# Optimization experiments

Hardware: AMD Instinct MI355X
Metric: run time of the kernel (lower is better)

The kernel has to match this reference:

```python
import jax, jax.numpy as jnp
import numpy as np

B, NT, NZ, CIN, H, DOUT, L = 16, 128, 256, 3, 64, 128, 3
N = NT * NZ  # 32768 nodes
EPS = 1e-5


def _build_edges():
    # Toroidal grid: each node connects to 4 neighbors (wrap-around in theta and zeta).
    T, Z = np.meshgrid(np.arange(NT), np.arange(NZ), indexing='ij')
    curr = (T * NZ + Z).ravel()
    nbrs = np.stack([
        (((T + 1) % NT) * NZ + Z).ravel(),
        (((T - 1) % NT) * NZ + Z).ravel(),
        (T * NZ + (Z + 1) % NZ).ravel(),
        (T * NZ + (Z - 1) % NZ).ravel(),
    ], axis=1)
    src = np.repeat(curr, 4)
    dst = nbrs.ravel()
    return np.stack([src, dst]).astype(np.int32)  # (2, 4N)


def setup_inputs() -> dict:
    key = jax.random.key(0)
    ks = jax.random.split(key, 8)
    s = lambda k, shp, fan: jax.random.normal(k, shp, jnp.float32) / np.float32(np.sqrt(fan))
    return {
        'x': jax.random.normal(ks[0], (B, CIN, N), jnp.float32),
        'edge_index': jnp.asarray(_build_edges()),
        'embed_W': s(ks[1], (CIN, H), CIN),
        'embed_b': jnp.zeros((H,), jnp.float32),
        'mp_W1': s(ks[2], (L, 2 * H, H), 2 * H),
        'mp_b1': jnp.zeros((L, H), jnp.float32),
        'mp_g1': jnp.ones((L, H), jnp.float32),
        'mp_be1': jnp.zeros((L, H), jnp.float32),
        'mp_W2': s(ks[3], (L, H, H), H),
        'mp_b2': jnp.zeros((L, H), jnp.float32),
        'mp_g2': jnp.ones((L, H), jnp.float32),
        'mp_be2': jnp.zeros((L, H), jnp.float32),
        'head_W1': s(ks[4], (H, H), H),
        'head_b1': jnp.zeros((H,), jnp.float32),
        'head_W2': s(ks[5], (H, DOUT), H),
        'head_b2': jnp.zeros((DOUT,), jnp.float32),
    }


def _bn(y, g, b):
    # BatchNorm1d in training mode: biased batch stats over (batch*nodes).
    m = y.mean(axis=(0, 1))
    v = y.var(axis=(0, 1))
    return (y - m) * (g * jax.lax.rsqrt(v + EPS)) + b


def reference(x, edge_index, embed_W, embed_b, mp_W1, mp_b1, mp_g1, mp_be1,
              mp_W2, mp_b2, mp_g2, mp_be2, head_W1, head_b1, head_W2, head_b2):
    src, dst = edge_index[0], edge_index[1]
    # embedding: (B,3,N) -> (B,N,H)
    h = jax.nn.relu(jnp.einsum('bcn,ch->bnh', x, embed_W) + embed_b)
    deg = jnp.zeros((N,), x.dtype).at[dst].add(1.0)
    deg = jnp.clip(deg, 1.0)[None, :, None]  # (1,N,1), all 4 on this graph
    for l in range(L):
        # gather neighbor features and scatter-add to destination, mean aggregate
        agg = jnp.zeros_like(h).at[:, dst, :].add(h[:, src, :]) / deg
        comb = jnp.concatenate([h, agg], axis=-1)  # (B,N,2H)
        y = jax.nn.relu(_bn(comb @ mp_W1[l] + mp_b1[l], mp_g1[l], mp_be1[l]))
        y = jax.nn.relu(_bn(y @ mp_W2[l] + mp_b2[l], mp_g2[l], mp_be2[l]))
        h = y + h  # residual (c_in == c_out)
    pooled = h.mean(axis=1)  # AdaptiveAvgPool1d(1) over nodes
    return jax.nn.relu(pooled @ head_W1 + head_b1) @ head_W2 + head_b2
```

## Files before the change

kernel.cpp:

```cpp
#include <hip/hip_runtime.h>

typedef unsigned short u16;
typedef u16 u16x8 __attribute__((ext_vector_type(8)));
typedef short s16x8 __attribute__((ext_vector_type(8)));
typedef float f32x4 __attribute__((ext_vector_type(4)));

#define NNODES 32768
#define EPSV 1e-5f
#define INV_ROWS (1.0f / 524288.0f)

__device__ __forceinline__ float bf2f(u16 u) {
  union { unsigned int i; float f; } v; v.i = ((unsigned int)u) << 16; return v.f;
}
__device__ __forceinline__ u16 f2bf(float f) {
  union { float f; unsigned int i; } v; v.f = f;
  unsigned int r = v.i + 0x7FFFu + ((v.i >> 16) & 1u);
  return (u16)(r >> 16);
}

__global__ __launch_bounds__(256) void k_prep(
    const float* __restrict__ W1, const float* __restrict__ W2,
    u16* __restrict__ w1t, u16* __restrict__ w2t) {
  int idx = blockIdx.x * 256 + threadIdx.x;
  if (idx < 24576) {
    int l = idx >> 13, rem = idx & 8191;
    int n = rem >> 7, k = rem & 127;
    float w = W1[l * 8192 + k * 64 + n];
    if (k >= 64) w *= 0.25f;
    w1t[idx] = f2bf(w);
  } else {
    int idx2 = idx - 24576;
    if (idx2 < 12288) {
      int l = idx2 >> 12, rem = idx2 & 4095;
      int n = rem >> 6, k = rem & 63;
      w2t[idx2] = f2bf(W2[l * 4096 + k * 64 + n]);
    }
  }
}

__global__ __launch_bounds__(256) void k_embed(
    const float* __restrict__ x, const float* __restrict__ eW,
    const float* __restrict__ eb, u16* __restrict__ h) {
  int tid = threadIdx.x;
  int chunk = tid & 7;
  int r = blockIdx.x * 32 + (tid >> 3);
  int b = r >> 15;
  int n = r & 32767;
  const float* xb = x + (size_t)b * 3 * NNODES + n;
  float x0 = xb[0], x1 = xb[NNODES], x2 = xb[2 * NNODES];
  int c0 = chunk * 8;
  u16x8 ov;
#pragma unroll
  for (int j = 0; j < 8; ++j) {
    float acc = eb[c0 + j] + x0 * eW[c0 + j] + x1 * eW[64 + c0 + j] + x2 * eW[128 + c0 + j];
    ov[j] = f2bf(fmaxf(acc, 0.f));
  }
  *reinterpret_cast<u16x8*>(&h[(size_t)r * 64 + c0]) = ov;
}

#define RSTR 72
__global__ __launch_bounds__(256) void k_gemm1(
    const u16* __restrict__ h, u16* __restrict__ ybuf,
    const u16* __restrict__ w1t, const float* __restrict__ b1,
    float* __restrict__ sums) {
  __shared__ __align__(16) u16 s_self[130 * RSTR];
  __shared__ __align__(16) u16 s_tp[128 * RSTR];
  __shared__ __align__(16) u16 s_tm[128 * RSTR];
  __shared__ __align__(16) u16 t_s[4][16 * RSTR];
  __shared__ float stat_s[4][128];

  int tid = threadIdx.x;
  int wv = tid >> 6, ln = tid & 63, ln15 = ln & 15, quad = ln >> 4;
  int blk = blockIdx.x;
  int xcd = blk & 7;
  int j = blk >> 3;
  int b = j >> 5;
  int local = j & 31;
  int t = xcd * 16 + (local >> 1);
  int half = local & 1;
  int z0 = half * 128;
  const u16* hb = h + (((size_t)b) << 15) * 64;
  int tp = (t + 1) & 127, tm = (t + 127) & 127;

  s16x8 bfT[4][2], bfB[4][2];
#pragma unroll
  for (int c = 0; c < 4; ++c)
#pragma unroll
    for (int kk = 0; kk < 2; ++kk) {
      bfT[c][kk] = *reinterpret_cast<const s16x8*>(
          &w1t[(c * 16 + ln15) * 128 + kk * 32 + quad * 8]);
      bfB[c][kk] = *reinterpret_cast<const s16x8*>(
          &w1t[(c * 16 + ln15) * 128 + 64 + kk * 32 + quad * 8]);
    }

  {
    u16x8 va[7];
#pragma unroll
    for (int ii = 0; ii < 7; ++ii) {
      int i = tid + ii * 256;
      int c = i & 7;
      int r = (i >= 1040) ? ((i - 1040) >> 3) : (i >> 3);
      int ring_t = (i >= 1040) ? tp : t;
      int z = (i >= 1040) ? (z0 + r) : ((z0 + 255 + r) & 255);
      va[ii] = *reinterpret_cast<const u16x8*>(&hb[((size_t)(ring_t * 256 + z)) * 64 + c * 8]);
    }
#pragma unroll
    for (int ii = 0; ii < 7; ++ii) {
      int i = tid + ii * 256;
      int c = i & 7;
      if (i < 1040) {
        *reinterpret_cast<u16x8*>(&s_self[(i >> 3) * RSTR + c * 8]) = va[ii];
      } else {
        *reinterpret_cast<u16x8*>(&s_tp[((i - 1040) >> 3) * RSTR + c * 8]) = va[ii];
      }
    }
    u16x8 vb[6];
#pragma unroll
    for (int ii = 0; ii < 6; ++ii) {
      int i = tid + (ii + 7) * 256;
      if (i < 3088) {
        int c = i & 7;
        int r = (i < 2064) ? ((i - 1040) >> 3) : ((i - 2064) >> 3);
        int ring_t = (i < 2064) ? tp : tm;
        vb[ii] = *reinterpret_cast<const u16x8*>(
            &hb[((size_t)(ring_t * 256 + z0 + r)) * 64 + c * 8]);
      }
    }
#pragma unroll
    for (int ii = 0; ii < 6; ++ii) {
      int i = tid + (ii + 7) * 256;
      if (i < 3088) {
        int c = i & 7;
        if (i < 2064) {
          *reinterpret_cast<u16x8*>(&s_tp[((i - 1040) >> 3) * RSTR + c * 8]) = vb[ii];
        } else {
          *reinterpret_cast<u16x8*>(&s_tm[((i - 2064) >> 3) * RSTR + c * 8]) = vb[ii];
        }
      }
    }
  }

  float bias_c[4];
#pragma unroll
  for (int c = 0; c < 4; ++c) bias_c[c] = b1[c * 16 + ln15];

  __syncthreads();

  float ls[4] = {0.f, 0.f, 0.f, 0.f}, ls2[4] = {0.f, 0.f, 0.f, 0.f};
  u16* ts = &t_s[wv][0];
  int cA = quad * 8;

#pragma unroll
  for (int st = 0; st < 2; ++st) {
    int row0 = st * 64 + wv * 16;
    int lr = row0 + ln15;

    s16x8 s0  = *reinterpret_cast<const s16x8*>(&s_self[(lr + 1) * RSTR + cA]);
    s16x8 s1  = *reinterpret_cast<const s16x8*>(&s_self[(lr + 1) * RSTR + 32 + cA]);
    s16x8 n0a = *reinterpret_cast<const s16x8*>(&s_tp[lr * RSTR + cA]);
    s16x8 n0b = *reinterpret_cast<const s16x8*>(&s_tp[lr * RSTR + 32 + cA]);
    s16x8 n1a = *reinterpret_cast<const s16x8*>(&s_tm[lr * RSTR + cA]);
    s16x8 n1b = *reinterpret_cast<const s16x8*>(&s_tm[lr * RSTR + 32 + cA]);
    s16x8 n2a = *reinterpret_cast<const s16x8*>(&s_self[(lr + 2) * RSTR + cA]);
    s16x8 n2b = *reinterpret_cast<const s16x8*>(&s_self[(lr + 2) * RSTR + 32 + cA]);
    s16x8 n3a = *reinterpret_cast<const s16x8*>(&s_self[lr * RSTR + cA]);
    s16x8 n3b = *reinterpret_cast<const s16x8*>(&s_self[lr * RSTR + 32 + cA]);

    f32x4 acc[4];
#pragma unroll
    for (int c = 0; c < 4; ++c) acc[c] = (f32x4){0.f, 0.f, 0.f, 0.f};
#pragma unroll
    for (int c = 0; c < 4; ++c) {
      acc[c] = __builtin_amdgcn_mfma_f32_16x16x32_bf16(s0,  bfT[c][0], acc[c], 0, 0, 0);
      acc[c] = __builtin_amdgcn_mfma_f32_16x16x32_bf16(s1,  bfT[c][1], acc[c], 0, 0, 0);
      acc[c] = __builtin_amdgcn_mfma_f32_16x16x32_bf16(n0a, bfB[c][0], acc[c], 0, 0, 0);
      acc[c] = __builtin_amdgcn_mfma_f32_16x16x32_bf16(n0b, bfB[c][1], acc[c], 0, 0, 0);
      acc[c] = __builtin_amdgcn_mfma_f32_16x16x32_bf16(n1a, bfB[c][0], acc[c], 0, 0, 0);
      acc[c] = __builtin_amdgcn_mfma_f32_16x16x32_bf16(n1b, bfB[c][1], acc[c], 0, 0, 0);
      acc[c] = __builtin_amdgcn_mfma_f32_16x16x32_bf16(n2a, bfB[c][0], acc[c], 0, 0, 0);
      acc[c] = __builtin_amdgcn_mfma_f32_16x16x32_bf16(n2b, bfB[c][1], acc[c], 0, 0, 0);
      acc[c] = __builtin_amdgcn_mfma_f32_16x16x32_bf16(n3a, bfB[c][0], acc[c], 0, 0, 0);
      acc[c] = __builtin_amdgcn_mfma_f32_16x16x32_bf16(n3b, bfB[c][1], acc[c], 0, 0, 0);
    }

    __builtin_amdgcn_wave_barrier();
#pragma unroll
    for (int c = 0; c < 4; ++c)
#pragma unroll
      for (int rg = 0; rg < 4; ++rg) {
        float vy = acc[c][rg] + bias_c[c];
        ls[c] += vy;
        ls2[c] += vy * vy;
        ts[(quad * 4 + rg) * RSTR + c * 16 + ln15] = f2bf(vy);
      }
    __builtin_amdgcn_wave_barrier();
    size_t R0 = (((size_t)b) << 15) + (size_t)t * 256 + z0 + row0;
    int lr2 = ln >> 2;
#pragma unroll
    for (int p = 0; p < 2; ++p) {
      int ck = (ln & 3) + p * 4;
      u16x8 v = *reinterpret_cast<const u16x8*>(&ts[lr2 * RSTR + ck * 8]);
      *reinterpret_cast<u16x8*>(&ybuf[(R0 + lr2) * 64 + ck * 8]) = v;
    }
    __builtin_amdgcn_wave_barrier();
  }

#pragma unroll
  for (int c = 0; c < 4; ++c) {
    ls[c]  += __shfl_xor(ls[c], 16, 64);  ls[c]  += __shfl_xor(ls[c], 32, 64);
    ls2[c] += __shfl_xor(ls2[c], 16, 64); ls2[c] += __shfl_xor(ls2[c], 32, 64);
  }
  if (ln < 16) {
#pragma unroll
    for (int c = 0; c < 4; ++c) {
      stat_s[wv][c * 16 + ln] = ls[c];
      stat_s[wv][64 + c * 16 + ln] = ls2[c];
    }
  }
  __syncthreads();
  if (tid < 128) {
    float s = stat_s[0][tid] + stat_s[1][tid] + stat_s[2][tid] + stat_s[3][tid];
    atomicAdd(&sums[xcd * 128 + tid], s);
  }
}

__global__ __launch_bounds__(256) void k_gemm2(
    u16* __restrict__ ybuf, const u16* __restrict__ w2t,
    const float* __restrict__ b2, const float* __restrict__ sums1,
    const float* __restrict__ g1, const float* __restrict__ be1,
    float* __restrict__ sums2) {
  __shared__ __align__(16) u16 t_s[4][16 * RSTR];
  __shared__ float s1_s[64], sh1_s[64];
  __shared__ float stat_s[4][128];

  int tid = threadIdx.x;
  int wv = tid >> 6, ln = tid & 63, ln15 = ln & 15, quad = ln >> 4;

  if (tid < 64) {
    float s = 0.f, s2 = 0.f;
#pragma unroll
    for (int sl = 0; sl < 8; ++sl) { s += sums1[sl * 128 + tid]; s2 += sums1[sl * 128 + 64 + tid]; }
    float m = s * INV_ROWS;
    float v = s2 * INV_ROWS - m * m;
    float sc = g1[tid] * rsqrtf(v + EPSV);
    s1_s[tid] = sc;
    sh1_s[tid] = be1[tid] - m * sc;
  }

  s16x8 bf[4][2];
#pragma unroll
  for (int c = 0; c < 4; ++c)
#pragma unroll
    for (int kk = 0; kk < 2; ++kk)
      bf[c][kk] = *reinterpret_cast<const s16x8*>(
          &w2t[(c * 16 + ln15) * 64 + kk * 32 + quad * 8]);

  float bias_c[4];
#pragma unroll
  for (int c = 0; c < 4; ++c) bias_c[c] = b2[c * 16 + ln15];

  __syncthreads();

  float sA[2][8], shA[2][8];
#pragma unroll
  for (int kk = 0; kk < 2; ++kk)
#pragma unroll
    for (int j = 0; j < 8; ++j) {
      int ch = kk * 32 + quad * 8 + j;
      sA[kk][j] = s1_s[ch];
      shA[kk][j] = sh1_s[ch];
    }

  float ls[4] = {0.f, 0.f, 0.f, 0.f}, ls2[4] = {0.f, 0.f, 0.f, 0.f};
  u16* ts = &t_s[wv][0];

  auto ld2 = [&](int it, u16x8* Y) {
    size_t row = (size_t)blockIdx.x * 256 + it * 64 + wv * 16 + ln15;
    Y[0] = *reinterpret_cast<const u16x8*>(&ybuf[row * 64 + quad * 8]);
    Y[1] = *reinterpret_cast<const u16x8*>(&ybuf[row * 64 + 32 + quad * 8]);
  };

  auto consume2 = [&](int it, u16x8* Y) {
    s16x8 a0, a1;
#pragma unroll
    for (int j = 0; j < 8; ++j) {
      a0[j] = (short)f2bf(fmaxf(bf2f(Y[0][j]) * sA[0][j] + shA[0][j], 0.f));
      a1[j] = (short)f2bf(fmaxf(bf2f(Y[1][j]) * sA[1][j] + shA[1][j], 0.f));
    }
    f32x4 acc[4];
#pragma unroll
    for (int c = 0; c < 4; ++c) acc[c] = (f32x4){0.f, 0.f, 0.f, 0.f};
#pragma unroll
    for (int c = 0; c < 4; ++c) {
      acc[c] = __builtin_amdgcn_mfma_f32_16x16x32_bf16(a0, bf[c][0], acc[c], 0, 0, 0);
      acc[c] = __builtin_amdgcn_mfma_f32_16x16x32_bf16(a1, bf[c][1], acc[c], 0, 0, 0);
    }
    __builtin_amdgcn_wave_barrier();
#pragma unroll
    for (int c = 0; c < 4; ++c)
#pragma unroll
      for (int rg = 0; rg < 4; ++rg) {
        float vy = acc[c][rg] + bias_c[c];
        ls[c] += vy;
        ls2[c] += vy * vy;
        ts[(quad * 4 + rg) * RSTR + c * 16 + ln15] = f2bf(vy);
      }
    __builtin_amdgcn_wave_barrier();
    size_t r0 = (size_t)blockIdx.x * 256 + it * 64 + wv * 16;
    int lr = ln >> 2;
#pragma unroll
    for (int p = 0; p < 2; ++p) {
      int ck = (ln & 3) + p * 4;
      u16x8 v = *reinterpret_cast<const u16x8*>(&ts[lr * RSTR + ck * 8]);
      *reinterpret_cast<u16x8*>(&ybuf[(r0 + lr) * 64 + ck * 8]) = v;
    }
    __builtin_amdgcn_wave_barrier();
  };

  u16x8 YA[2], YB[2];
  ld2(0, YA);
#pragma unroll 1
  for (int it = 0; it < 4; it += 2) {
    ld2(it + 1, YB);
    consume2(it, YA);
    if (it + 2 < 4) ld2(it + 2, YA);
    consume2(it + 1, YB);
  }

#pragma unroll
  for (int c = 0; c < 4; ++c) {
    ls[c]  += __shfl_xor(ls[c], 16, 64);  ls[c]  += __shfl_xor(ls[c], 32, 64);
    ls2[c] += __shfl_xor(ls2[c], 16, 64); ls2[c] += __shfl_xor(ls2[c], 32, 64);
  }
  if (ln < 16) {
#pragma unroll
    for (int c = 0; c < 4; ++c) {
      stat_s[wv][c * 16 + ln] = ls[c];
      stat_s[wv][64 + c * 16 + ln] = ls2[c];
    }
  }
  __syncthreads();
  if (tid < 128) {
    float s = stat_s[0][tid] + stat_s[1][tid] + stat_s[2][tid] + stat_s[3][tid];
    atomicAdd(&sums2[(blockIdx.x & 7) * 128 + tid], s);
  }
}

__global__ __launch_bounds__(256) void k_resid(
    u16* __restrict__ h, const u16* __restrict__ zbuf,
    const float* __restrict__ sums2, const float* __restrict__ g2,
    const float* __restrict__ be2, float* __restrict__ pooled) {
  __shared__ float s2_s[64], sh2_s[64];
  __shared__ float red_s[32][68];
  int tid = threadIdx.x;
  if (tid < 64) {
    float s = 0.f, s2 = 0.f;
#pragma unroll
    for (int sl = 0; sl < 8; ++sl) { s += sums2[sl * 128 + tid]; s2 += sums2[sl * 128 + 64 + tid]; }
    float m = s * INV_ROWS;
    float v = s2 * INV_ROWS - m * m;
    float sc = g2[tid] * rsqrtf(v + EPSV);
    s2_s[tid] = sc;
    sh2_s[tid] = be2[tid] - m * sc;
  }
  __syncthreads();
  int ch0 = (tid & 7) * 8;
  float scl[8], shl[8];
#pragma unroll
  for (int j = 0; j < 8; ++j) { scl[j] = s2_s[ch0 + j]; shl[j] = sh2_s[ch0 + j]; }
  float p[8] = {0.f, 0.f, 0.f, 0.f, 0.f, 0.f, 0.f, 0.f};
  size_t base0 = (size_t)blockIdx.x * 16384 + tid * 8;
#pragma unroll 1
  for (int it = 0; it < 8; it += 2) {
    size_t ba = base0 + it * 2048;
    size_t bb = ba + 2048;
    u16x8 zva = *reinterpret_cast<const u16x8*>(&zbuf[ba]);
    u16x8 hva = *reinterpret_cast<const u16x8*>(&h[ba]);
    u16x8 zvb = *reinterpret_cast<const u16x8*>(&zbuf[bb]);
    u16x8 hvb = *reinterpret_cast<const u16x8*>(&h[bb]);
    u16x8 ova, ovb;
#pragma unroll
    for (int j = 0; j < 8; ++j) {
      float a = fmaxf(bf2f(zva[j]) * scl[j] + shl[j], 0.f);
      float nh = bf2f(hva[j]) + a;
      ova[j] = f2bf(nh);
      p[j] += bf2f(ova[j]);
    }
    *reinterpret_cast<u16x8*>(&h[ba]) = ova;
#pragma unroll
    for (int j = 0; j < 8; ++j) {
      float a = fmaxf(bf2f(zvb[j]) * scl[j] + shl[j], 0.f);
      float nh = bf2f(hvb[j]) + a;
      ovb[j] = f2bf(nh);
      p[j] += bf2f(ovb[j]);
    }
    *reinterpret_cast<u16x8*>(&h[bb]) = ovb;
  }
  if (pooled != nullptr) {
    int g = tid >> 3;
#pragma unroll
    for (int j = 0; j < 8; ++j) red_s[g][ch0 + j] = p[j];
    __syncthreads();
    if (tid < 64) {
      float s = 0.f;
#pragma unroll
      for (int gg = 0; gg < 32; ++gg) s += red_s[gg][tid];
      atomicAdd(&pooled[(blockIdx.x >> 7) * 64 + tid], s);
    }
  }
}

__global__ __launch_bounds__(256) void k_head(
    const float* __restrict__ pooled, const float* __restrict__ hW1,
    const float* __restrict__ hb1, const float* __restrict__ hW2,
    const float* __restrict__ hb2, float* __restrict__ out) {
  __shared__ float p_s[16 * 64];
  __shared__ float t1_s[16 * 64];
  int tid = threadIdx.x;
#pragma unroll
  for (int j = 0; j < 4; ++j)
    p_s[tid + 256 * j] = pooled[tid + 256 * j] * (1.0f / 32768.0f);
  __syncthreads();
#pragma unroll
  for (int j = 0; j < 4; ++j) {
    int idx = tid + 256 * j;
    int bb = idx >> 6, o = idx & 63;
    float acc = hb1[o];
    for (int k = 0; k < 64; ++k) acc += p_s[bb * 64 + k] * hW1[k * 64 + o];
    t1_s[idx] = fmaxf(acc, 0.f);
  }
  __syncthreads();
#pragma unroll
  for (int j = 0; j < 8; ++j) {
    int idx = tid + 256 * j;
    int bb = idx >> 7, o = idx & 127;
    float acc = hb2[o];
    for (int k = 0; k < 64; ++k) acc += t1_s[bb * 64 + k] * hW2[k * 128 + o];
    out[idx] = acc;
  }
}

extern "C" void kernel_launch(void* const* d_in, const int* in_sizes, int n_in,
                              void* d_out, int out_size, void* d_ws, size_t ws_size,
                              hipStream_t stream) {
  const float* x   = (const float*)d_in[0];
  const float* eW  = (const float*)d_in[2];
  const float* eb  = (const float*)d_in[3];
  const float* W1  = (const float*)d_in[4];
  const float* b1  = (const float*)d_in[5];
  const float* g1  = (const float*)d_in[6];
  const float* be1 = (const float*)d_in[7];
  const float* W2  = (const float*)d_in[8];
  const float* b2  = (const float*)d_in[9];
  const float* g2  = (const float*)d_in[10];
  const float* be2 = (const float*)d_in[11];
  const float* hW1 = (const float*)d_in[12];
  const float* hb1 = (const float*)d_in[13];
  const float* hW2 = (const float*)d_in[14];
  const float* hb2 = (const float*)d_in[15];
  float* out = (float*)d_out;

  char* ws = (char*)d_ws;
  u16* h    = (u16*)ws;
  u16* ybuf = (u16*)(ws + 67108864);
  float* stats  = (float*)(ws + 134217728);
  float* pooled = stats + 6144;
  u16* w1t = (u16*)(ws + 134217728 + 7168 * 4);
  u16* w2t = w1t + 24576;

  hipMemsetAsync(stats, 0, (6144 + 1024) * sizeof(float), stream);

  k_prep<<<144, 256, 0, stream>>>(W1, W2, w1t, w2t);
  k_embed<<<16384, 256, 0, stream>>>(x, eW, eb, h);
  for (int l = 0; l < 3; ++l) {
    float* sum1 = stats + l * 2048;
    float* sum2 = stats + l * 2048 + 1024;
    k_gemm1<<<4096, 256, 0, stream>>>(h, ybuf, w1t + l * 8192, b1 + l * 64, sum1);
    k_gemm2<<<2048, 256, 0, stream>>>(ybuf, w2t + l * 4096, b2 + l * 64,
                                      sum1, g1 + l * 64, be1 + l * 64, sum2);
    k_resid<<<2048, 256, 0, stream>>>(h, ybuf, sum2, g2 + l * 64, be2 + l * 64,
                                      (l == 2) ? pooled : nullptr);
  }
  k_head<<<1, 256, 0, stream>>>(pooled, hW1, hb1, hW2, hb2, out);
}
```

Measured before the change: 472.6 us.

## Halve gemm1 tile to 64 nodes per block and skip final-layer h writeback

Each gemm1 block now handles 64 z-positions instead of 128, with twice as many blocks launched and about half the shared memory per block. This should raise occupancy and parallelism, but each block reloads a 2-row halo for proportionally fewer output rows. Separately, the last residual layer no longer writes h back to global memory, because only the pooled sums are consumed afterwards. That removes a full write of the activation tensor.

```diff
diff --git a/kernel.cpp b/kernel.cpp
--- a/kernel.cpp
+++ b/kernel.cpp
@@ -63,9 +63,9 @@
     const u16* __restrict__ h, u16* __restrict__ ybuf,
     const u16* __restrict__ w1t, const float* __restrict__ b1,
     float* __restrict__ sums) {
-  __shared__ __align__(16) u16 s_self[130 * RSTR];
-  __shared__ __align__(16) u16 s_tp[128 * RSTR];
-  __shared__ __align__(16) u16 s_tm[128 * RSTR];
+  __shared__ __align__(16) u16 s_self[66 * RSTR];
+  __shared__ __align__(16) u16 s_tp[64 * RSTR];
+  __shared__ __align__(16) u16 s_tm[64 * RSTR];
   __shared__ __align__(16) u16 t_s[4][16 * RSTR];
   __shared__ float stat_s[4][128];
 
@@ -74,11 +74,11 @@
   int blk = blockIdx.x;
   int xcd = blk & 7;
   int j = blk >> 3;
-  int b = j >> 5;
-  int local = j & 31;
-  int t = xcd * 16 + (local >> 1);
-  int half = local & 1;
-  int z0 = half * 128;
+  int b = j >> 6;
+  int local = j & 63;
+  int t = xcd * 16 + (local >> 2);
+  int q = local & 3;
+  int z0 = q * 64;
   const u16* hb = h + (((size_t)b) << 15) * 64;
   int tp = (t + 1) & 127, tm = (t + 127) & 127;
 
@@ -98,43 +98,27 @@
 #pragma unroll
     for (int ii = 0; ii < 7; ++ii) {
       int i = tid + ii * 256;
-      int c = i & 7;
-      int r = (i >= 1040) ? ((i - 1040) >> 3) : (i >> 3);
-      int ring_t = (i >= 1040) ? tp : t;
-      int z = (i >= 1040) ? (z0 + r) : ((z0 + 255 + r) & 255);
-      va[ii] = *reinterpret_cast<const u16x8*>(&hb[((size_t)(ring_t * 256 + z)) * 64 + c * 8]);
+      if (i < 1552) {
+        int c = i & 7;
+        int r, ring_t, z;
+        if (i < 528)       { r = i >> 3;          ring_t = t;  z = (z0 + 255 + r) & 255; }
+        else if (i < 1040) { r = (i - 528) >> 3;  ring_t = tp; z = z0 + r; }
+        else               { r = (i - 1040) >> 3; ring_t = tm; z = z0 + r; }
+        va[ii] = *reinterpret_cast<const u16x8*>(
+            &hb[((size_t)(ring_t * 256 + z)) * 64 + c * 8]);
+      }
     }
 #pragma unroll
     for (int ii = 0; ii < 7; ++ii) {
       int i = tid + ii * 256;
-      int c = i & 7;
-      if (i < 1040) {
-        *reinterpret_cast<u16x8*>(&s_self[(i >> 3) * RSTR + c * 8]) = va[ii];
-      } else {
-        *reinterpret_cast<u16x8*>(&s_tp[((i - 1040) >> 3) * RSTR + c * 8]) = va[ii];
-      }
-    }
-    u16x8 vb[6];
-#pragma unroll
-    for (int ii = 0; ii < 6; ++ii) {
-      int i = tid + (ii + 7) * 256;
-      if (i < 3088) {
+      if (i < 1552) {
         int c = i & 7;
-        int r = (i < 2064) ? ((i - 1040) >> 3) : ((i - 2064) >> 3);
-        int ring_t = (i < 2064) ? tp : tm;
-        vb[ii] = *reinterpret_cast<const u16x8*>(
-            &hb[((size_t)(ring_t * 256 + z0 + r)) * 64 + c * 8]);
-      }
-    }
-#pragma unroll
-    for (int ii = 0; ii < 6; ++ii) {
-      int i = tid + (ii + 7) * 256;
-      if (i < 3088) {
-        int c = i & 7;
-        if (i < 2064) {
-          *reinterpret_cast<u16x8*>(&s_tp[((i - 1040) >> 3) * RSTR + c * 8]) = vb[ii];
+        if (i < 528) {
+          *reinterpret_cast<u16x8*>(&s_self[(i >> 3) * RSTR + c * 8]) = va[ii];
+        } else if (i < 1040) {
+          *reinterpret_cast<u16x8*>(&s_tp[((i - 528) >> 3) * RSTR + c * 8]) = va[ii];
         } else {
-          *reinterpret_cast<u16x8*>(&s_tm[((i - 2064) >> 3) * RSTR + c * 8]) = vb[ii];
+          *reinterpret_cast<u16x8*>(&s_tm[((i - 1040) >> 3) * RSTR + c * 8]) = va[ii];
         }
       }
     }
@@ -146,55 +130,54 @@
 
   __syncthreads();
 
-  float ls[4] = {0.f, 0.f, 0.f, 0.f}, ls2[4] = {0.f, 0.f, 0.f, 0.f};
+  float ls[4], ls2[4];
   u16* ts = &t_s[wv][0];
   int cA = quad * 8;
-
-#pragma unroll
-  for (int st = 0; st < 2; ++st) {
-    int row0 = st * 64 + wv * 16;
-    int lr = row0 + ln15;
-
-    s16x8 s0  = *reinterpret_cast<const s16x8*>(&s_self[(lr + 1) * RSTR + cA]);
-    s16x8 s1  = *reinterpret_cast<const s16x8*>(&s_self[(lr + 1) * RSTR + 32 + cA]);
-    s16x8 n0a = *reinterpret_cast<const s16x8*>(&s_tp[lr * RSTR + cA]);
-    s16x8 n0b = *reinterpret_cast<const s16x8*>(&s_tp[lr * RSTR + 32 + cA]);
-    s16x8 n1a = *reinterpret_cast<const s16x8*>(&s_tm[lr * RSTR + cA]);
-    s16x8 n1b = *reinterpret_cast<const s16x8*>(&s_tm[lr * RSTR + 32 + cA]);
-    s16x8 n2a = *reinterpret_cast<const s16x8*>(&s_self[(lr + 2) * RSTR + cA]);
-    s16x8 n2b = *reinterpret_cast<const s16x8*>(&s_self[(lr + 2) * RSTR + 32 + cA]);
-    s16x8 n3a = *reinterpret_cast<const s16x8*>(&s_self[lr * RSTR + cA]);
-    s16x8 n3b = *reinterpret_cast<const s16x8*>(&s_self[lr * RSTR + 32 + cA]);
-
-    f32x4 acc[4];
-#pragma unroll
-    for (int c = 0; c < 4; ++c) acc[c] = (f32x4){0.f, 0.f, 0.f, 0.f};
-#pragma unroll
-    for (int c = 0; c < 4; ++c) {
-      acc[c] = __builtin_amdgcn_mfma_f32_16x16x32_bf16(s0,  bfT[c][0], acc[c], 0, 0, 0);
-      acc[c] = __builtin_amdgcn_mfma_f32_16x16x32_bf16(s1,  bfT[c][1], acc[c], 0, 0, 0);
-      acc[c] = __builtin_amdgcn_mfma_f32_16x16x32_bf16(n0a, bfB[c][0], acc[c], 0, 0, 0);
-      acc[c] = __builtin_amdgcn_mfma_f32_16x16x32_bf16(n0b, bfB[c][1], acc[c], 0, 0, 0);
-      acc[c] = __builtin_amdgcn_mfma_f32_16x16x32_bf16(n1a, bfB[c][0], acc[c], 0, 0, 0);
-      acc[c] = __builtin_amdgcn_mfma_f32_16x16x32_bf16(n1b, bfB[c][1], acc[c], 0, 0, 0);
-      acc[c] = __builtin_amdgcn_mfma_f32_16x16x32_bf16(n2a, bfB[c][0], acc[c], 0, 0, 0);
-      acc[c] = __builtin_amdgcn_mfma_f32_16x16x32_bf16(n2b, bfB[c][1], acc[c], 0, 0, 0);
-      acc[c] = __builtin_amdgcn_mfma_f32_16x16x32_bf16(n3a, bfB[c][0], acc[c], 0, 0, 0);
-      acc[c] = __builtin_amdgcn_mfma_f32_16x16x32_bf16(n3b, bfB[c][1], acc[c], 0, 0, 0);
-    }
-
-    __builtin_amdgcn_wave_barrier();
-#pragma unroll
-    for (int c = 0; c < 4; ++c)
-#pragma unroll
-      for (int rg = 0; rg < 4; ++rg) {
-        float vy = acc[c][rg] + bias_c[c];
-        ls[c] += vy;
-        ls2[c] += vy * vy;
-        ts[(quad * 4 + rg) * RSTR + c * 16 + ln15] = f2bf(vy);
-      }
-    __builtin_amdgcn_wave_barrier();
-    size_t R0 = (((size_t)b) << 15) + (size_t)t * 256 + z0 + row0;
+  int lr = wv * 16 + ln15;
+
+  s16x8 s0  = *reinterpret_cast<const s16x8*>(&s_self[(lr + 1) * RSTR + cA]);
+  s16x8 s1  = *reinterpret_cast<const s16x8*>(&s_self[(lr + 1) * RSTR + 32 + cA]);
+  s16x8 n0a = *reinterpret_cast<const s16x8*>(&s_tp[lr * RSTR + cA]);
+  s16x8 n0b = *reinterpret_cast<const s16x8*>(&s_tp[lr * RSTR + 32 + cA]);
+  s16x8 n1a = *reinterpret_cast<const s16x8*>(&s_tm[lr * RSTR + cA]);
+  s16x8 n1b = *reinterpret_cast<const s16x8*>(&s_tm[lr * RSTR + 32 + cA]);
+  s16x8 n2a = *reinterpret_cast<const s16x8*>(&s_self[(lr + 2) * RSTR + cA]);
+  s16x8 n2b = *reinterpret_cast<const s16x8*>(&s_self[(lr + 2) * RSTR + 32 + cA]);
+  s16x8 n3a = *reinterpret_cast<const s16x8*>(&s_self[lr * RSTR + cA]);
+  s16x8 n3b = *reinterpret_cast<const s16x8*>(&s_self[lr * RSTR + 32 + cA]);
+
+  f32x4 acc[4];
+#pragma unroll
+  for (int c = 0; c < 4; ++c) acc[c] = (f32x4){0.f, 0.f, 0.f, 0.f};
+#pragma unroll
+  for (int c = 0; c < 4; ++c) {
+    acc[c] = __builtin_amdgcn_mfma_f32_16x16x32_bf16(s0,  bfT[c][0], acc[c], 0, 0, 0);
+    acc[c] = __builtin_amdgcn_mfma_f32_16x16x32_bf16(s1,  bfT[c][1], acc[c], 0, 0, 0);
+    acc[c] = __builtin_amdgcn_mfma_f32_16x16x32_bf16(n0a, bfB[c][0], acc[c], 0, 0, 0);
+    acc[c] = __builtin_amdgcn_mfma_f32_16x16x32_bf16(n0b, bfB[c][1], acc[c], 0, 0, 0);
+    acc[c] = __builtin_amdgcn_mfma_f32_16x16x32_bf16(n1a, bfB[c][0], acc[c], 0, 0, 0);
+    acc[c] = __builtin_amdgcn_mfma_f32_16x16x32_bf16(n1b, bfB[c][1], acc[c], 0, 0, 0);
+    acc[c] = __builtin_amdgcn_mfma_f32_16x16x32_bf16(n2a, bfB[c][0], acc[c], 0, 0, 0);
+    acc[c] = __builtin_amdgcn_mfma_f32_16x16x32_bf16(n2b, bfB[c][1], acc[c], 0, 0, 0);
+    acc[c] = __builtin_amdgcn_mfma_f32_16x16x32_bf16(n3a, bfB[c][0], acc[c], 0, 0, 0);
+    acc[c] = __builtin_amdgcn_mfma_f32_16x16x32_bf16(n3b, bfB[c][1], acc[c], 0, 0, 0);
+  }
+
+  __builtin_amdgcn_wave_barrier();
+#pragma unroll
+  for (int c = 0; c < 4; ++c) {
+    ls[c] = 0.f; ls2[c] = 0.f;
+#pragma unroll
+    for (int rg = 0; rg < 4; ++rg) {
+      float vy = acc[c][rg] + bias_c[c];
+      ls[c] += vy;
+      ls2[c] += vy * vy;
+      ts[(quad * 4 + rg) * RSTR + c * 16 + ln15] = f2bf(vy);
+    }
+  }
+  __builtin_amdgcn_wave_barrier();
+  {
+    size_t R0 = (((size_t)b) << 15) + (size_t)t * 256 + z0 + wv * 16;
     int lr2 = ln >> 2;
 #pragma unroll
     for (int p = 0; p < 2; ++p) {
@@ -202,7 +185,6 @@
       u16x8 v = *reinterpret_cast<const u16x8*>(&ts[lr2 * RSTR + ck * 8]);
       *reinterpret_cast<u16x8*>(&ybuf[(R0 + lr2) * 64 + ck * 8]) = v;
     }
-    __builtin_amdgcn_wave_barrier();
   }
 
 #pragma unroll
@@ -369,6 +351,7 @@
 #pragma unroll
   for (int j = 0; j < 8; ++j) { scl[j] = s2_s[ch0 + j]; shl[j] = sh2_s[ch0 + j]; }
   float p[8] = {0.f, 0.f, 0.f, 0.f, 0.f, 0.f, 0.f, 0.f};
+  bool do_pool = (pooled != nullptr);
   size_t base0 = (size_t)blockIdx.x * 16384 + tid * 8;
 #pragma unroll 1
   for (int it = 0; it < 8; it += 2) {
@@ -382,21 +365,21 @@
 #pragma unroll
     for (int j = 0; j < 8; ++j) {
       float a = fmaxf(bf2f(zva[j]) * scl[j] + shl[j], 0.f);
-      float nh = bf2f(hva[j]) + a;
-      ova[j] = f2bf(nh);
+      ova[j] = f2bf(bf2f(hva[j]) + a);
       p[j] += bf2f(ova[j]);
     }
-    *reinterpret_cast<u16x8*>(&h[ba]) = ova;
 #pragma unroll
     for (int j = 0; j < 8; ++j) {
       float a = fmaxf(bf2f(zvb[j]) * scl[j] + shl[j], 0.f);
-      float nh = bf2f(hvb[j]) + a;
-      ovb[j] = f2bf(nh);
+      ovb[j] = f2bf(bf2f(hvb[j]) + a);
       p[j] += bf2f(ovb[j]);
     }
-    *reinterpret_cast<u16x8*>(&h[bb]) = ovb;
-  }
-  if (pooled != nullptr) {
+    if (!do_pool) {
+      *reinterpret_cast<u16x8*>(&h[ba]) = ova;
+      *reinterpret_cast<u16x8*>(&h[bb]) = ovb;
+    }
+  }
+  if (do_pool) {
     int g = tid >> 3;
 #pragma unroll
     for (int j = 0; j < 8; ++j) red_s[g][ch0 + j] = p[j];
@@ -475,7 +458,7 @@
   for (int l = 0; l < 3; ++l) {
     float* sum1 = stats + l * 2048;
     float* sum2 = stats + l * 2048 + 1024;
-    k_gemm1<<<4096, 256, 0, stream>>>(h, ybuf, w1t + l * 8192, b1 + l * 64, sum1);
+    k_gemm1<<<8192, 256, 0, stream>>>(h, ybuf, w1t + l * 8192, b1 + l * 64, sum1);
     k_gemm2<<<2048, 256, 0, stream>>>(ybuf, w2t + l * 4096, b2 + l * 64,
                                       sum1, g1 + l * 64, be1 + l * 64, sum2);
     k_resid<<<2048, 256, 0, stream>>>(h, ybuf, sum2, g2 + l * 64, be2 + l * 64,
```

After: 531.8 us. +12.5%, slower.
